# Kernel tuning notes

Hardware: AMD Instinct MI355X
Metric: run time of the kernel (lower is better)

## Reference

```python
import jax, jax.numpy as jnp
import numpy as np

SEQ, HID = 4096, 1024
NEG_INF = -10000000000.0


def setup_inputs() -> dict:
    key = jax.random.key(0)
    ks = jax.random.split(key, 6)
    s = 1.0 / np.sqrt(HID)
    return {
        "query": jax.random.normal(ks[0], (SEQ, HID), jnp.float32),
        "key": jax.random.normal(ks[1], (SEQ, HID), jnp.float32),
        "value": jax.random.normal(ks[2], (SEQ, HID), jnp.float32),
        # SASRec causal mask: allowed positions are 1, masked are 0
        "mask": jnp.tril(jnp.ones((SEQ, SEQ), jnp.int32)),
        "Wq": jax.random.normal(ks[3], (HID, HID), jnp.float32) * s,
        "Wk": jax.random.normal(ks[4], (HID, HID), jnp.float32) * s,
        "Wv": jax.random.normal(ks[5], (HID, HID), jnp.float32) * s,
    }


def reference(query, key, value, mask, Wq, Wk, Wv):
    # nn.Linear(bias=False): y = x @ W.T
    Q = query @ Wq.T   # [S, H]
    K = key @ Wk.T     # [S, H]
    V = value @ Wv.T   # [S, H]
    scale = jnp.sqrt(jnp.asarray(HID, Q.dtype))
    energy = (Q @ K.T) / scale                      # [S, S]
    energy = jnp.where(mask == 0, NEG_INF, energy)  # masked_fill
    attention = jax.nn.softmax(energy, axis=-1)     # [S, S]
    x = attention @ V                               # dropout is identity in eval
    return (x, attention)
```

## Files before the change

kernel.cpp:

```cpp
#include <hip/hip_runtime.h>

#define SEQ 4096
#define HID 1024

typedef _Float16 f16x4 __attribute__((ext_vector_type(4)));
typedef _Float16 f16x8 __attribute__((ext_vector_type(8)));
typedef float    f32x4 __attribute__((ext_vector_type(4)));

__device__ __forceinline__ void gld16(const void* g, void* l) {
    __builtin_amdgcn_global_load_lds(
        (const __attribute__((address_space(1))) unsigned int*)g,
        (__attribute__((address_space(3))) unsigned int*)l, 16, 0, 0);
}

__global__ __launch_bounds__(256) void cast_all(
    const float4* __restrict__ q, const float4* __restrict__ k,
    const float4* __restrict__ v,
    const float4* __restrict__ wq, const float4* __restrict__ wk,
    const float4* __restrict__ wv,
    f16x4* __restrict__ qh, f16x4* __restrict__ kh, f16x4* __restrict__ vh,
    f16x4* __restrict__ wqh, f16x4* __restrict__ wkh, f16x4* __restrict__ wvh,
    int nX4, int nW4) {
    int t = blockIdx.x * 256 + threadIdx.x;
    const float4 *a, *b, *c; f16x4 *da, *db, *dc; int idx;
    if (t < nX4) { a = q; b = k; c = v; da = qh; db = kh; dc = vh; idx = t; }
    else if (t < nX4 + nW4) {
        idx = t - nX4;
        a = wq; b = wk; c = wv; da = wqh; db = wkh; dc = wvh;
    } else return;
    float4 va = a[idx], vb = b[idx], vc = c[idx];
    f16x4 oa = {(_Float16)va.x, (_Float16)va.y, (_Float16)va.z, (_Float16)va.w};
    f16x4 ob = {(_Float16)vb.x, (_Float16)vb.y, (_Float16)vb.z, (_Float16)vb.w};
    f16x4 oc = {(_Float16)vc.x, (_Float16)vc.y, (_Float16)vc.z, (_Float16)vc.w};
    da[idx] = oa; db[idx] = ob; dc[idx] = oc;
}

template <typename OutT, bool TRI_SKIP, bool TRI_K, int ZMODE>
__global__ __launch_bounds__(256) void gemm_nt(
    const _Float16* __restrict__ A, const _Float16* __restrict__ Bt,
    OutT* __restrict__ C, int M, int N, int K, float scale,
    long sA, long sB, long sC, int KC, float* __restrict__ PB,
    const _Float16* __restrict__ A2, const _Float16* __restrict__ B2,
    OutT* __restrict__ C2, int N2) {
    __shared__ __attribute__((aligned(16))) _Float16 As[2 * 128 * 32];
    __shared__ __attribute__((aligned(16))) _Float16 Bs[2 * 128 * 32];

    int bm = blockIdx.y;
    int bn = blockIdx.x;
    if (TRI_SKIP && bn > bm) return;
    const _Float16* Ap = A;
    const _Float16* Bp = Bt;
    OutT* Cp = C;
    int Nloc = N;
    if (ZMODE == 7) {
        if (blockIdx.z < 2) {
            Ap = A  + (long)blockIdx.z * sA;
            Bp = Bt + (long)blockIdx.z * sB;
            Cp = C  + (long)blockIdx.z * sC;
        } else {
            Ap = A2; Bp = B2; Cp = C2; Nloc = N2;
            bm = blockIdx.x; bn = blockIdx.y;
        }
    }

    int kstart = 0, kend, zslot = -1;
    if (ZMODE == 4) {
        const int y = 79 - (int)blockIdx.y;
        int g = 0;
        while (4 * (g + 1) * (g + 2) <= y) ++g;
        const int rem = y - 4 * g * (g + 1);
        const int m   = g + 1;
        const int rg  = rem / m;
        bm = 8 * g + rg;
        const int z = rem - rg * m;
        kstart = z * KC;
        kend   = min((bm + 1) * 128, kstart + KC);
        if (z > 0) zslot = 4 * g * (g - 1) + rg * g + (z - 1);
    } else if (ZMODE == 5) {
        kstart = blockIdx.z * KC;
        kend   = kstart + KC;
        Cp += (long)blockIdx.z * sC;
    } else {
        kend = TRI_K ? min(K, (bm + 1) * 128) : K;
    }

    const int tid = threadIdx.x;
    const int tr  = tid >> 2;
    const int tc8 = (tid & 3) * 8;
    const int tcs8 = (((tid & 3) ^ (tr & 3))) * 8;

    const _Float16* Ab = Ap + (size_t)bm * 128 * K;
    const _Float16* Bb = Bp + (size_t)bn * 128 * K;

    const int wave = tid >> 6;
    const int lane = tid & 63;
    const int wm = (wave >> 1) * 64;
    const int wn = (wave & 1) * 64;
    const int lr = lane & 15;
    const int lks = (((lane >> 4) ^ (lane & 3))) * 8;

    f32x4 acc[4][4];
#pragma unroll
    for (int i = 0; i < 4; ++i)
#pragma unroll
        for (int j = 0; j < 4; ++j) acc[i][j] = (f32x4)0.0f;

    #define STAGE(b, kk)                                                        \
        do {                                                                    \
            const int off_ = (b) * 4096;                                        \
            gld16(Ab + (size_t)tr * K        + (kk) + tcs8,                     \
                  &As[off_ + tr * 32 + tc8]);                                   \
            gld16(Ab + (size_t)(64 + tr) * K + (kk) + tcs8,                     \
                  &As[off_ + (64 + tr) * 32 + tc8]);                            \
            gld16(Bb + (size_t)tr * K        + (kk) + tcs8,                     \
                  &Bs[off_ + tr * 32 + tc8]);                                   \
            gld16(Bb + (size_t)(64 + tr) * K + (kk) + tcs8,                     \
                  &Bs[off_ + (64 + tr) * 32 + tc8]);                            \
        } while (0)

    const int nit = (kend - kstart) >> 5;
    STAGE(0, kstart);
    for (int it = 0; it < nit; ++it) {
        const int cur = it & 1;
        if (it + 1 < nit) {
            STAGE(cur ^ 1, kstart + (it + 1) * 32);
            asm volatile("s_waitcnt vmcnt(4)" ::: "memory");
        } else {
            asm volatile("s_waitcnt vmcnt(0)" ::: "memory");
        }
        __builtin_amdgcn_s_barrier();

        const int off = cur * 4096;
        f16x8 af[4], bfr[4];
#pragma unroll
        for (int i = 0; i < 4; ++i)
            af[i] = *(const f16x8*)&As[off + (wm + i * 16 + lr) * 32 + lks];
#pragma unroll
        for (int j = 0; j < 4; ++j)
            bfr[j] = *(const f16x8*)&Bs[off + (wn + j * 16 + lr) * 32 + lks];
#pragma unroll
        for (int i = 0; i < 4; ++i)
#pragma unroll
            for (int j = 0; j < 4; ++j)
                acc[i][j] = __builtin_amdgcn_mfma_f32_16x16x32_f16(
                    af[i], bfr[j], acc[i][j], 0, 0, 0);
        __builtin_amdgcn_s_barrier();
    }
    #undef STAGE

    const int er = (lane >> 4) * 4;
    const int ec = lane & 15;
#pragma unroll
    for (int i = 0; i < 4; ++i) {
#pragma unroll
        for (int j = 0; j < 4; ++j) {
            const int lrow0 = wm + i * 16 + er;
            const int col   = bn * 128 + wn + j * 16 + ec;
#pragma unroll
            for (int r = 0; r < 4; ++r) {
                const float val = acc[i][j][r] * scale;
                if (ZMODE == 4 && zslot >= 0)
                    PB[(size_t)(zslot * 128 + lrow0 + r) * 1024 + col] = val;
                else
                    Cp[(long)(bm * 128 + lrow0 + r) * Nloc + col] = (OutT)val;
            }
        }
    }
}

__global__ __launch_bounds__(256) void reduce_pv(
    float* __restrict__ out, const float* __restrict__ PB) {
    const int row = 1024 + blockIdx.x;
    const int bm  = row >> 7;
    const int g   = bm >> 3;
    const int slot0 = 4 * g * (g - 1) + (bm - 8 * g) * g;
    const int rloc  = row & 127;
    float4* o = (float4*)(out + (size_t)row * 1024) + threadIdx.x;
    float4 acc = *o;
    for (int z = 0; z < g; ++z) {
        const float4 p = *((const float4*)(PB +
            ((size_t)(slot0 + z) * 128 + rloc) * 1024) + threadIdx.x);
        acc.x += p.x; acc.y += p.y; acc.z += p.z; acc.w += p.w;
    }
    *o = acc;
}

__global__ __launch_bounds__(256) void softmax_causal(
    _Float16* __restrict__ EP0, const _Float16* __restrict__ EP1,
    float* __restrict__ att, int S) {
    __shared__ float rowbuf[SEQ];
    __shared__ float red[8];
    const int i   = blockIdx.x;
    const int tid = threadIdx.x;
    const int wv  = tid >> 6, ln = tid & 63;
    _Float16* E0row = EP0 + (size_t)i * S;
    const _Float16* E1row = EP1 + (size_t)i * S;

    float lmax = -INFINITY;
    for (int j8 = tid * 8; j8 <= i; j8 += 2048) {
        f16x8 a8 = *(const f16x8*)&E0row[j8];
        f16x8 b8 = *(const f16x8*)&E1row[j8];
#pragma unroll
        for (int u = 0; u < 8; ++u) {
            int j = j8 + u;
            if (j <= i) {
                float vv = (float)a8[u] + (float)b8[u];
                rowbuf[j] = vv;
                lmax = fmaxf(lmax, vv);
            }
        }
    }
#pragma unroll
    for (int o = 32; o > 0; o >>= 1) lmax = fmaxf(lmax, __shfl_down(lmax, o, 64));
    if (ln == 0) red[wv] = lmax;
    __syncthreads();
    if (tid == 0)
        red[4] = fmaxf(fmaxf(red[0], red[1]), fmaxf(red[2], red[3]));
    __syncthreads();
    const float rmax = red[4];

    float lsum = 0.0f;
    for (int j4 = tid * 4; j4 <= i; j4 += 1024) {
        float4 e = *(float4*)&rowbuf[j4];
        float4 o;
        o.x = (j4     <= i) ? __expf(e.x - rmax) : 0.f;
        o.y = (j4 + 1 <= i) ? __expf(e.y - rmax) : 0.f;
        o.z = (j4 + 2 <= i) ? __expf(e.z - rmax) : 0.f;
        o.w = (j4 + 3 <= i) ? __expf(e.w - rmax) : 0.f;
        *(float4*)&rowbuf[j4] = o;
        lsum += o.x + o.y + o.z + o.w;
    }
#pragma unroll
    for (int o = 32; o > 0; o >>= 1) lsum += __shfl_down(lsum, o, 64);
    __syncthreads();
    if (ln == 0) red[wv] = lsum;
    __syncthreads();
    if (tid == 0)
        red[4] = red[0] + red[1] + red[2] + red[3];
    __syncthreads();
    const float rinv = 1.0f / red[4];

    float* arow = att + (size_t)i * S;
    const int jlim = ((i >> 7) + 1) << 7;
    for (int j4 = tid * 4; j4 < S; j4 += 1024) {
        float4 a;
        a.x = (j4     <= i) ? rowbuf[j4]     * rinv : 0.f;
        a.y = (j4 + 1 <= i) ? rowbuf[j4 + 1] * rinv : 0.f;
        a.z = (j4 + 2 <= i) ? rowbuf[j4 + 2] * rinv : 0.f;
        a.w = (j4 + 3 <= i) ? rowbuf[j4 + 3] * rinv : 0.f;
        *(float4*)&arow[j4] = a;
        if (j4 < jlim) {
            f16x4 p = {(_Float16)a.x, (_Float16)a.y, (_Float16)a.z, (_Float16)a.w};
            *(f16x4*)&E0row[j4] = p;
        }
    }
}

extern "C" void kernel_launch(void* const* d_in, const int* in_sizes, int n_in,
                              void* d_out, int out_size, void* d_ws, size_t ws_size,
                              hipStream_t stream) {
    const float* q  = (const float*)d_in[0];
    const float* k  = (const float*)d_in[1];
    const float* v  = (const float*)d_in[2];
    const float* Wq = (const float*)d_in[4];
    const float* Wk = (const float*)d_in[5];
    const float* Wv = (const float*)d_in[6];

    float* out_x   = (float*)d_out;
    float* out_att = out_x + (size_t)SEQ * HID;

    char* ws = (char*)d_ws;
    const size_t SH = (size_t)SEQ * HID * sizeof(_Float16);
    const size_t HH = (size_t)HID * HID * sizeof(_Float16);
    _Float16* qh  = (_Float16*)(ws);
    _Float16* vh  = (_Float16*)(ws + SH);
    _Float16* wqh = (_Float16*)(ws + 2 * SH);
    _Float16* wkh = (_Float16*)(ws + 2 * SH + HH);
    _Float16* wvh = (_Float16*)(ws + 2 * SH + 2 * HH);
    _Float16* EP1 = (_Float16*)(ws);
    _Float16* kh  = (_Float16*)(ws + 4 * SH);
    _Float16* Qh  = (_Float16*)(ws + 5 * SH);
    _Float16* Kh  = (_Float16*)(ws + 6 * SH);
    _Float16* VT  = (_Float16*)(ws + 7 * SH);
    _Float16* EP0 = (_Float16*)(ws + 8 * SH);
    float* Pbuf = (float*)ws;

    const int nX4 = SEQ * HID / 4, nW4 = HID * HID / 4;
    cast_all<<<(nX4 + nW4 + 255) / 256, 256, 0, stream>>>(
        (const float4*)q, (const float4*)k, (const float4*)v,
        (const float4*)Wq, (const float4*)Wk, (const float4*)Wv,
        (f16x4*)qh, (f16x4*)kh, (f16x4*)vh,
        (f16x4*)wqh, (f16x4*)wkh, (f16x4*)wvh, nX4, nW4);

    gemm_nt<_Float16, false, false, 7><<<dim3(HID / 128, SEQ / 128, 3), 256, 0, stream>>>(
        qh, wqh, Qh, SEQ, HID, HID, 1.0f,
        (long)(kh - qh), (long)(wkh - wqh), (long)(Kh - Qh), 0, nullptr,
        wvh, vh, VT, SEQ);

    gemm_nt<_Float16, true, false, 5><<<dim3(SEQ / 128, SEQ / 128, 2), 256, 0, stream>>>(
        Qh, Kh, EP0, SEQ, SEQ, HID, 0.03125f,
        0, 0, (long)(EP1 - EP0), 512, nullptr, nullptr, nullptr, nullptr, 0);

    softmax_causal<<<SEQ, 256, 0, stream>>>(EP0, EP1, out_att, SEQ);

    gemm_nt<float, false, true, 4><<<dim3(HID / 128, 80), 256, 0, stream>>>(
        EP0, VT, out_x, SEQ, HID, SEQ, 1.0f, 0, 0, 0, 1024, Pbuf,
        nullptr, nullptr, nullptr, 0);

    reduce_pv<<<3072, 256, 0, stream>>>(out_x, Pbuf);
}
```

Baseline: 305.4 us.

## Replace split-K energy GEMM with triangular 1D grid and coarser PV split

The QK^T GEMM no longer runs as two K-halves summed in softmax. It now launches 528 blocks covering only the lower-triangular tiles with full-K accumulation, with ids swizzled to spread load. Softmax reads a single fp16 energy buffer. The PV split-K changes from up to 4 chunks per row block (KC=1024) to at most 2 (KC=2048), which cuts partial-buffer traffic and the reduction work. The V-projection block mapping is also remapped linearly. Fewer parallel blocks means each one carries longer-K work, which may hurt occupancy balance.

```diff
diff --git a/kernel.cpp b/kernel.cpp
--- a/kernel.cpp
+++ b/kernel.cpp
@@ -58,28 +58,29 @@
             Bp = Bt + (long)blockIdx.z * sB;
             Cp = C  + (long)blockIdx.z * sC;
         } else {
+            const int lin = (int)blockIdx.y * 8 + (int)blockIdx.x;
             Ap = A2; Bp = B2; Cp = C2; Nloc = N2;
-            bm = blockIdx.x; bn = blockIdx.y;
-        }
+            bm = lin & 7; bn = lin >> 3;
+        }
+    }
+    if (ZMODE == 8) {
+        const int id = (int)blockIdx.x;
+        const int y  = (id & 7) * 66 + (id >> 3);
+        int g = 0;
+        while ((g + 1) * (g + 2) / 2 <= y) ++g;
+        bm = g;
+        bn = y - g * (g + 1) / 2;
     }
 
     int kstart = 0, kend, zslot = -1;
     if (ZMODE == 4) {
-        const int y = 79 - (int)blockIdx.y;
-        int g = 0;
-        while (4 * (g + 1) * (g + 2) <= y) ++g;
-        const int rem = y - 4 * g * (g + 1);
-        const int m   = g + 1;
-        const int rg  = rem / m;
-        bm = 8 * g + rg;
-        const int z = rem - rg * m;
+        const int y = 47 - (int)blockIdx.y;
+        int z;
+        if (y < 16) { bm = y; z = 0; }
+        else { const int r = y - 16; bm = 16 + (r >> 1); z = r & 1; }
         kstart = z * KC;
         kend   = min((bm + 1) * 128, kstart + KC);
-        if (z > 0) zslot = 4 * g * (g - 1) + rg * g + (z - 1);
-    } else if (ZMODE == 5) {
-        kstart = blockIdx.z * KC;
-        kend   = kstart + KC;
-        Cp += (long)blockIdx.z * sC;
+        if (z == 1) zslot = bm - 16;
     } else {
         kend = TRI_K ? min(K, (bm + 1) * 128) : K;
     }
@@ -170,41 +171,33 @@
 
 __global__ __launch_bounds__(256) void reduce_pv(
     float* __restrict__ out, const float* __restrict__ PB) {
-    const int row = 1024 + blockIdx.x;
-    const int bm  = row >> 7;
-    const int g   = bm >> 3;
-    const int slot0 = 4 * g * (g - 1) + (bm - 8 * g) * g;
-    const int rloc  = row & 127;
+    const int row  = 2048 + blockIdx.x;
+    const int slot = (row >> 7) - 16;
     float4* o = (float4*)(out + (size_t)row * 1024) + threadIdx.x;
-    float4 acc = *o;
-    for (int z = 0; z < g; ++z) {
-        const float4 p = *((const float4*)(PB +
-            ((size_t)(slot0 + z) * 128 + rloc) * 1024) + threadIdx.x);
-        acc.x += p.x; acc.y += p.y; acc.z += p.z; acc.w += p.w;
-    }
-    *o = acc;
+    const float4 p = *((const float4*)(PB +
+        ((size_t)slot * 128 + (row & 127)) * 1024) + threadIdx.x);
+    float4 a = *o;
+    a.x += p.x; a.y += p.y; a.z += p.z; a.w += p.w;
+    *o = a;
 }
 
 __global__ __launch_bounds__(256) void softmax_causal(
-    _Float16* __restrict__ EP0, const _Float16* __restrict__ EP1,
-    float* __restrict__ att, int S) {
+    _Float16* __restrict__ EP, float* __restrict__ att, int S) {
     __shared__ float rowbuf[SEQ];
     __shared__ float red[8];
     const int i   = blockIdx.x;
     const int tid = threadIdx.x;
     const int wv  = tid >> 6, ln = tid & 63;
-    _Float16* E0row = EP0 + (size_t)i * S;
-    const _Float16* E1row = EP1 + (size_t)i * S;
+    _Float16* Erow = EP + (size_t)i * S;
 
     float lmax = -INFINITY;
     for (int j8 = tid * 8; j8 <= i; j8 += 2048) {
-        f16x8 a8 = *(const f16x8*)&E0row[j8];
-        f16x8 b8 = *(const f16x8*)&E1row[j8];
+        f16x8 e8 = *(const f16x8*)&Erow[j8];
 #pragma unroll
         for (int u = 0; u < 8; ++u) {
             int j = j8 + u;
             if (j <= i) {
-                float vv = (float)a8[u] + (float)b8[u];
+                float vv = (float)e8[u];
                 rowbuf[j] = vv;
                 lmax = fmaxf(lmax, vv);
             }
@@ -251,7 +244,7 @@
         *(float4*)&arow[j4] = a;
         if (j4 < jlim) {
             f16x4 p = {(_Float16)a.x, (_Float16)a.y, (_Float16)a.z, (_Float16)a.w};
-            *(f16x4*)&E0row[j4] = p;
+            *(f16x4*)&Erow[j4] = p;
         }
     }
 }
@@ -277,7 +270,6 @@
     _Float16* wqh = (_Float16*)(ws + 2 * SH);
     _Float16* wkh = (_Float16*)(ws + 2 * SH + HH);
     _Float16* wvh = (_Float16*)(ws + 2 * SH + 2 * HH);
-    _Float16* EP1 = (_Float16*)(ws);
     _Float16* kh  = (_Float16*)(ws + 4 * SH);
     _Float16* Qh  = (_Float16*)(ws + 5 * SH);
     _Float16* Kh  = (_Float16*)(ws + 6 * SH);
@@ -297,15 +289,15 @@
         (long)(kh - qh), (long)(wkh - wqh), (long)(Kh - Qh), 0, nullptr,
         wvh, vh, VT, SEQ);
 
-    gemm_nt<_Float16, true, false, 5><<<dim3(SEQ / 128, SEQ / 128, 2), 256, 0, stream>>>(
+    gemm_nt<_Float16, false, false, 8><<<528, 256, 0, stream>>>(
         Qh, Kh, EP0, SEQ, SEQ, HID, 0.03125f,
-        0, 0, (long)(EP1 - EP0), 512, nullptr, nullptr, nullptr, nullptr, 0);
-
-    softmax_causal<<<SEQ, 256, 0, stream>>>(EP0, EP1, out_att, SEQ);
-
-    gemm_nt<float, false, true, 4><<<dim3(HID / 128, 80), 256, 0, stream>>>(
-        EP0, VT, out_x, SEQ, HID, SEQ, 1.0f, 0, 0, 0, 1024, Pbuf,
+        0, 0, 0, 0, nullptr, nullptr, nullptr, nullptr, 0);
+
+    softmax_causal<<<SEQ, 256, 0, stream>>>(EP0, out_att, SEQ);
+
+    gemm_nt<float, false, true, 4><<<dim3(HID / 128, 48), 256, 0, stream>>>(
+        EP0, VT, out_x, SEQ, HID, SEQ, 1.0f, 0, 0, 0, 2048, Pbuf,
         nullptr, nullptr, nullptr, 0);
 
-    reduce_pv<<<3072, 256, 0, stream>>>(out_x, Pbuf);
-}
+    reduce_pv<<<2048, 256, 0, stream>>>(out_x, Pbuf);
+}
```

Result: no change. 300.4 us (-1.6%).

## Replace split-K QK^T with a lower-triangular 1D grid and drop partial merge

Applied to the files above, without the earlier changes.

The QK^T GEMM no longer splits K into two halves written to separate fp16 buffers. It now launches 528 blocks, one per lower-triangular 128x128 tile, mapped through a triangular index with an interleaved ordering, and each block does the full K=1024. The softmax then reads a single energy buffer instead of summing two partials, which removes an extra read stream and the second output write. The V projection's block index mapping is also reordered. The cost is fewer blocks in flight (528 vs 1024 launched, with no early-return waste) and longer per-block K loops.

```diff
diff --git a/kernel.cpp b/kernel.cpp
--- a/kernel.cpp
+++ b/kernel.cpp
@@ -58,9 +58,18 @@
             Bp = Bt + (long)blockIdx.z * sB;
             Cp = C  + (long)blockIdx.z * sC;
         } else {
+            const int lin = (int)blockIdx.y * 8 + (int)blockIdx.x;
             Ap = A2; Bp = B2; Cp = C2; Nloc = N2;
-            bm = blockIdx.x; bn = blockIdx.y;
-        }
+            bm = lin & 7; bn = lin >> 3;
+        }
+    }
+    if (ZMODE == 8) {
+        const int id = (int)blockIdx.x;
+        const int y  = (id & 7) * 66 + (id >> 3);
+        int g = 0;
+        while ((g + 1) * (g + 2) / 2 <= y) ++g;
+        bm = g;
+        bn = y - g * (g + 1) / 2;
     }
 
     int kstart = 0, kend, zslot = -1;
@@ -76,10 +85,6 @@
         kstart = z * KC;
         kend   = min((bm + 1) * 128, kstart + KC);
         if (z > 0) zslot = 4 * g * (g - 1) + rg * g + (z - 1);
-    } else if (ZMODE == 5) {
-        kstart = blockIdx.z * KC;
-        kend   = kstart + KC;
-        Cp += (long)blockIdx.z * sC;
     } else {
         kend = TRI_K ? min(K, (bm + 1) * 128) : K;
     }
@@ -186,25 +191,22 @@
 }
 
 __global__ __launch_bounds__(256) void softmax_causal(
-    _Float16* __restrict__ EP0, const _Float16* __restrict__ EP1,
-    float* __restrict__ att, int S) {
+    _Float16* __restrict__ EP, float* __restrict__ att, int S) {
     __shared__ float rowbuf[SEQ];
     __shared__ float red[8];
     const int i   = blockIdx.x;
     const int tid = threadIdx.x;
     const int wv  = tid >> 6, ln = tid & 63;
-    _Float16* E0row = EP0 + (size_t)i * S;
-    const _Float16* E1row = EP1 + (size_t)i * S;
+    _Float16* Erow = EP + (size_t)i * S;
 
     float lmax = -INFINITY;
     for (int j8 = tid * 8; j8 <= i; j8 += 2048) {
-        f16x8 a8 = *(const f16x8*)&E0row[j8];
-        f16x8 b8 = *(const f16x8*)&E1row[j8];
+        f16x8 e8 = *(const f16x8*)&Erow[j8];
 #pragma unroll
         for (int u = 0; u < 8; ++u) {
             int j = j8 + u;
             if (j <= i) {
-                float vv = (float)a8[u] + (float)b8[u];
+                float vv = (float)e8[u];
                 rowbuf[j] = vv;
                 lmax = fmaxf(lmax, vv);
             }
@@ -251,7 +253,7 @@
         *(float4*)&arow[j4] = a;
         if (j4 < jlim) {
             f16x4 p = {(_Float16)a.x, (_Float16)a.y, (_Float16)a.z, (_Float16)a.w};
-            *(f16x4*)&E0row[j4] = p;
+            *(f16x4*)&Erow[j4] = p;
         }
     }
 }
@@ -277,7 +279,6 @@
     _Float16* wqh = (_Float16*)(ws + 2 * SH);
     _Float16* wkh = (_Float16*)(ws + 2 * SH + HH);
     _Float16* wvh = (_Float16*)(ws + 2 * SH + 2 * HH);
-    _Float16* EP1 = (_Float16*)(ws);
     _Float16* kh  = (_Float16*)(ws + 4 * SH);
     _Float16* Qh  = (_Float16*)(ws + 5 * SH);
     _Float16* Kh  = (_Float16*)(ws + 6 * SH);
@@ -297,11 +298,11 @@
         (long)(kh - qh), (long)(wkh - wqh), (long)(Kh - Qh), 0, nullptr,
         wvh, vh, VT, SEQ);
 
-    gemm_nt<_Float16, true, false, 5><<<dim3(SEQ / 128, SEQ / 128, 2), 256, 0, stream>>>(
+    gemm_nt<_Float16, false, false, 8><<<528, 256, 0, stream>>>(
         Qh, Kh, EP0, SEQ, SEQ, HID, 0.03125f,
-        0, 0, (long)(EP1 - EP0), 512, nullptr, nullptr, nullptr, nullptr, 0);
-
-    softmax_causal<<<SEQ, 256, 0, stream>>>(EP0, EP1, out_att, SEQ);
+        0, 0, 0, 0, nullptr, nullptr, nullptr, nullptr, 0);
+
+    softmax_causal<<<SEQ, 256, 0, stream>>>(EP0, out_att, SEQ);
 
     gemm_nt<float, false, true, 4><<<dim3(HID / 128, 80), 256, 0, stream>>>(
         EP0, VT, out_x, SEQ, HID, SEQ, 1.0f, 0, 0, 0, 1024, Pbuf,
```

After: 289.9 us. -5.1%, faster.
